# Optimization experiments

Hardware: AMD Instinct MI355X
Metric: run time of the kernel (lower is better)

Reference implementation:

```python
import jax, jax.numpy as jnp
import numpy as np

VTH = 1.0          # firing threshold
SG_ALPHA = 4.0     # surrogate-gradient sharpness
TAU_MEM = 20.0

@jax.custom_vjp
def spike_fn(v):
    # Heaviside spike: 1 where membrane exceeds 0 (v is already v_mem - VTH)
    return (v > 0.0).astype(v.dtype)

def _spike_fwd(v):
    return spike_fn(v), v

def _spike_bwd(v, g):
    # sigmoid surrogate derivative: alpha * s * (1 - s)
    s = jax.nn.sigmoid(SG_ALPHA * v)
    return (g * SG_ALPHA * s * (1.0 - s),)

spike_fn.defvjp(_spike_fwd, _spike_bwd)

def lif_scan(h):
    # h: (batch, time, seq, hidden) -> spikes same shape, rate scalar
    beta = 1.0 - 1.0 / TAU_MEM  # membrane decay
    b, t, s, d = h.shape
    h_t = jnp.moveaxis(h, 1, 0)  # (time, batch, seq, hidden)

    def step(v, inp):
        v = beta * v + inp
        spk = spike_fn(v - VTH)
        v = v * (1.0 - spk)  # hard reset
        return v, spk

    v0 = jnp.zeros((b, s, d), dtype=h.dtype)
    _, spikes = jax.lax.scan(step, v0, h_t)
    spikes = jnp.moveaxis(spikes, 0, 1)  # (batch, time, seq, hidden)
    rate = spikes.mean()
    return spikes, rate

def setup_inputs() -> dict:
    key = jax.random.key(0)
    k1, k2, k3 = jax.random.split(key, 3)
    b, t, s, d = 16, 4, 256, 512
    hidden = 2048
    x = jax.random.normal(k1, (b, t, s, d), dtype=jnp.float32)
    # Kaiming-ish init so membrane inputs are O(1)
    w1 = jax.random.normal(k2, (hidden, d), dtype=jnp.float32) * (1.0 / np.sqrt(d))
    w2 = jax.random.normal(k3, (d, hidden), dtype=jnp.float32) * (1.0 / np.sqrt(hidden))
    return {"x": x, "w1": w1, "w2": w2}

def reference(x, w1, w2):
    # fc1: (b,t,s,d) @ (hidden,d)^T -> (b,t,s,hidden)
    h = jnp.einsum('btsd,hd->btsh', x, w1)
    spikes, rate = lif_scan(h)
    # fc2: (b,t,s,hidden) @ (d,hidden)^T -> (b,t,s,d)
    out = jnp.einsum('btsh,dh->btsd', spikes, w2)
    return out, rate
```

## Files before the change

kernel.cpp:

```cpp
#include <hip/hip_runtime.h>
#include <stdint.h>


typedef __attribute__((ext_vector_type(8))) short short8;
typedef __attribute__((ext_vector_type(4))) float f32x4;

#define AS1 __attribute__((address_space(1)))
#define AS3 __attribute__((address_space(3)))

__device__ __forceinline__ void load_lds16(const void* g, void* l) {
  __builtin_amdgcn_global_load_lds((const AS1 void*)g, (AS3 void*)l, 16, 0, 0);
}

__device__ __forceinline__ unsigned short f2bf(float f) {
  union { float f; unsigned u; } un; un.f = f;
  unsigned r = un.u + 0x7FFF + ((un.u >> 16) & 1);
  return (unsigned short)(r >> 16);
}
__device__ __forceinline__ float bf2f(unsigned short u) {
  union { unsigned u; float f; } un; un.u = ((unsigned)u) << 16; return un.f;
}

__global__ __launch_bounds__(256) void k0_split(
    const float* __restrict__ w2, unsigned short* __restrict__ hi,
    unsigned short* __restrict__ lo)
{
  int i = (blockIdx.x * 256 + threadIdx.x) * 4;
  float4 w = *(const float4*)&w2[i];
  unsigned short h4[4], l4[4];
  float ws[4] = {w.x, w.y, w.z, w.w};
#pragma unroll
  for (int c = 0; c < 4; ++c) {
    unsigned short h = f2bf(ws[c]);
    h4[c] = h;
    l4[c] = f2bf(ws[c] - bf2f(h));
  }
  *(ushort4*)&hi[i] = *(const ushort4*)h4;
  *(ushort4*)&lo[i] = *(const ushort4*)l4;
}

#define K1KT 16
#define SA_STR 176
#define SB_STR 176

__global__ __launch_bounds__(256, 4) void k1_gemm_lif(
    const float* __restrict__ x,
    const float* __restrict__ w1,
    unsigned short* __restrict__ spikes,
    unsigned* __restrict__ cnt_out)
{
  __shared__ float sA[K1KT * SA_STR];
  __shared__ float sB[K1KT * SB_STR];

  const int tid = threadIdx.x;
  const int tx  = tid & 15;
  const int ty  = tid >> 4;

  const int bx = blockIdx.x;
  const int b  = bx >> 3;
  const int s0 = (bx & 7) * 32;
  const int h0 = blockIdx.y * 128;

  const int kg = tid & 3;
  const int u  = tid >> 2;

  float acc[8][8];
#pragma unroll
  for (int m = 0; m < 8; ++m)
#pragma unroll
    for (int j = 0; j < 8; ++j) acc[m][j] = 0.0f;

  const size_t growA0 = ((size_t)(b * 4 + (u & 3)) << 8) + s0 + (u >> 2);
  const size_t growA1 = growA0 + 16;
  const float* xA0 = x  + growA0 * 512 + kg * 4;
  const float* xA1 = x  + growA1 * 512 + kg * 4;
  const float* wB0 = w1 + (size_t)(h0 + u) * 512 + kg * 4;
  const float* wB1 = w1 + (size_t)(h0 + u + 64) * 512 + kg * 4;

  float* sAw = &sA[(4 * kg) * SA_STR + u + 16 * kg];
  float* sBw = &sB[(4 * kg) * SB_STR + u + 16 * kg];

  const float* sAr = &sA[ty * 8];
  const float* sBr = &sB[tx * 4];

  for (int k0 = 0; k0 < 512; k0 += K1KT) {
    float4 a0v = *(const float4*)(xA0 + k0);
    float4 a1v = *(const float4*)(xA1 + k0);
    float4 b0v = *(const float4*)(wB0 + k0);
    float4 b1v = *(const float4*)(wB1 + k0);

    __syncthreads();
    {
      float a0s[4] = {a0v.x, a0v.y, a0v.z, a0v.w};
      float a1s[4] = {a1v.x, a1v.y, a1v.z, a1v.w};
      float b0s[4] = {b0v.x, b0v.y, b0v.z, b0v.w};
      float b1s[4] = {b1v.x, b1v.y, b1v.z, b1v.w};
#pragma unroll
      for (int c = 0; c < 4; ++c) {
        sAw[c * SA_STR]      = a0s[c];
        sAw[c * SA_STR + 64] = a1s[c];
        sBw[c * SB_STR]      = b0s[c];
        sBw[c * SB_STR + 64] = b1s[c];
      }
    }
    __syncthreads();

#pragma unroll
    for (int k = 0; k < K1KT; ++k) {
      const int off = k * SA_STR + 16 * (k >> 2);
      float4 va0 = *(const float4*)(sAr + off);
      float4 va1 = *(const float4*)(sAr + off + 4);
      float4 vb0 = *(const float4*)(sBr + off);
      float4 vb1 = *(const float4*)(sBr + off + 64);
      float av[8] = {va0.x, va0.y, va0.z, va0.w, va1.x, va1.y, va1.z, va1.w};
      float bv[8] = {vb0.x, vb0.y, vb0.z, vb0.w, vb1.x, vb1.y, vb1.z, vb1.w};
#pragma unroll
      for (int m = 0; m < 8; ++m)
#pragma unroll
        for (int j = 0; j < 8; ++j)
          acc[m][j] = __builtin_fmaf(av[m], bv[j], acc[m][j]);
    }
  }

  unsigned cnt = 0;
#pragma unroll
  for (int i = 0; i < 2; ++i) {
    unsigned short sp[4][8];
#pragma unroll
    for (int j = 0; j < 8; ++j) {
      float v = 0.0f;
#pragma unroll
      for (int t = 0; t < 4; ++t) {
        float vv = __fadd_rn(__fmul_rn(0.95f, v), acc[i * 4 + t][j]);
        bool s = vv > 1.0f;
        sp[t][j] = s ? (unsigned short)0x3F80 : (unsigned short)0;
        cnt += s ? 1u : 0u;
        v = s ? 0.0f : vv;
      }
    }
#pragma unroll
    for (int t = 0; t < 4; ++t) {
      size_t grow = ((size_t)(b * 4 + t) << 8) + s0 + ty * 2 + i;
      unsigned short* rowp = spikes + grow * 2048 + h0;
      ushort4 o0, o1;
      o0.x = sp[t][0]; o0.y = sp[t][1]; o0.z = sp[t][2]; o0.w = sp[t][3];
      o1.x = sp[t][4]; o1.y = sp[t][5]; o1.z = sp[t][6]; o1.w = sp[t][7];
      *(ushort4*)&rowp[tx * 4]      = o0;
      *(ushort4*)&rowp[64 + tx * 4] = o1;
    }
  }

#pragma unroll
  for (int off = 32; off; off >>= 1) cnt += __shfl_down(cnt, off);
  if ((tid & 63) == 0) atomicAdd(cnt_out, cnt);
}

__global__ __launch_bounds__(256, 2) void k2_gemm_mfma(
    const unsigned short* __restrict__ spikes,
    const unsigned short* __restrict__ w2h,
    const unsigned short* __restrict__ w2l,
    float* __restrict__ out)
{
  __shared__ alignas(16) short smA [128 * 64];
  __shared__ alignas(16) short smBh[128 * 64];
  __shared__ alignas(16) short smBl[128 * 64];

  const int tid  = threadIdx.x;
  const int lane = tid & 63;
  const int quad = lane >> 4;
  const int l15  = lane & 15;
  const int wv   = tid >> 6;
  const int wm   = wv & 1;
  const int wn   = wv >> 1;

  const size_t r0 = (size_t)blockIdx.x * 128;
  const int    d0 = blockIdx.y * 128;

  int srow[4], sg8[4];
#pragma unroll
  for (int j = 0; j < 4; ++j) {
    int gi  = j * 256 + tid;
    srow[j] = gi >> 3;
    sg8[j]  = ((gi & 7) ^ (srow[j] & 7)) * 8;
  }

  const unsigned short* ab  = spikes + r0 * 2048;
  const unsigned short* bhb = w2h + (size_t)d0 * 2048;
  const unsigned short* blb = w2l + (size_t)d0 * 2048;

  f32x4 acc[4][4] = {};

  for (int k0 = 0; k0 < 2048; k0 += 64) {
    __syncthreads();
#pragma unroll
    for (int j = 0; j < 4; ++j) {
      load_lds16(ab  + (size_t)srow[j] * 2048 + k0 + sg8[j],
                 &smA [(j * 256 + tid) * 8]);
      load_lds16(bhb + (size_t)srow[j] * 2048 + k0 + sg8[j],
                 &smBh[(j * 256 + tid) * 8]);
      load_lds16(blb + (size_t)srow[j] * 2048 + k0 + sg8[j],
                 &smBl[(j * 256 + tid) * 8]);
    }
    __syncthreads();

#pragma unroll
    for (int ks = 0; ks < 2; ++ks) {
      short8 af[4], bh[4], bl[4];
#pragma unroll
      for (int mi = 0; mi < 4; ++mi) {
        int m = wm * 64 + mi * 16 + l15;
        af[mi] = ((const short8*)smA)[m * 8 + ((ks * 4 + quad) ^ (m & 7))];
      }
#pragma unroll
      for (int ni = 0; ni < 4; ++ni) {
        int n = wn * 64 + ni * 16 + l15;
        int sl = n * 8 + ((ks * 4 + quad) ^ (n & 7));
        bh[ni] = ((const short8*)smBh)[sl];
        bl[ni] = ((const short8*)smBl)[sl];
      }
#pragma unroll
      for (int mi = 0; mi < 4; ++mi)
#pragma unroll
        for (int ni = 0; ni < 4; ++ni) {
          acc[mi][ni] = __builtin_amdgcn_mfma_f32_16x16x32_bf16(
              af[mi], bh[ni], acc[mi][ni], 0, 0, 0);
          acc[mi][ni] = __builtin_amdgcn_mfma_f32_16x16x32_bf16(
              af[mi], bl[ni], acc[mi][ni], 0, 0, 0);
        }
    }
  }

  float* ob = out + r0 * 512 + d0;
#pragma unroll
  for (int mi = 0; mi < 4; ++mi)
#pragma unroll
    for (int ni = 0; ni < 4; ++ni)
#pragma unroll
      for (int r = 0; r < 4; ++r) {
        int rr = wm * 64 + mi * 16 + quad * 4 + r;
        int cc = wn * 64 + ni * 16 + l15;
        ob[(size_t)rr * 512 + cc] = acc[mi][ni][r];
      }
}

#define KT 16
#define PADF 68

__global__ __launch_bounds__(256) void k2_gemm_valu(
    const unsigned short* __restrict__ spikes,
    const float* __restrict__ w2,
    float* __restrict__ out)
{
  __shared__ float sA[KT][PADF];
  __shared__ float sB[KT][PADF];

  const int tid = threadIdx.x;
  const int tx  = tid & 15;
  const int ty  = tid >> 4;
  const int lr  = tid >> 2;
  const int lg  = tid & 3;

  const size_t r0 = (size_t)blockIdx.x * 64;
  const int    d0 = blockIdx.y * 64;

  float acc[4][4];
#pragma unroll
  for (int i = 0; i < 4; ++i)
#pragma unroll
    for (int j = 0; j < 4; ++j) acc[i][j] = 0.0f;

  for (int k0 = 0; k0 < 2048; k0 += KT) {
    __syncthreads();
    ushort4 av = *(const ushort4*)&spikes[(r0 + lr) * 2048 + k0 + lg * 4];
    float4  bv = *(const float4*)&w2[(size_t)(d0 + lr) * 2048 + k0 + lg * 4];
    sA[lg * 4 + 0][lr] = bf2f(av.x); sA[lg * 4 + 1][lr] = bf2f(av.y);
    sA[lg * 4 + 2][lr] = bf2f(av.z); sA[lg * 4 + 3][lr] = bf2f(av.w);
    sB[lg * 4 + 0][lr] = bv.x; sB[lg * 4 + 1][lr] = bv.y;
    sB[lg * 4 + 2][lr] = bv.z; sB[lg * 4 + 3][lr] = bv.w;
    __syncthreads();

#pragma unroll
    for (int k = 0; k < KT; ++k) {
      float4 a4 = *(const float4*)&sA[k][ty * 4];
      float4 b4 = *(const float4*)&sB[k][tx * 4];
      float aa[4] = {a4.x, a4.y, a4.z, a4.w};
      float bb[4] = {b4.x, b4.y, b4.z, b4.w};
#pragma unroll
      for (int i = 0; i < 4; ++i)
#pragma unroll
        for (int j = 0; j < 4; ++j)
          acc[i][j] = __builtin_fmaf(aa[i], bb[j], acc[i][j]);
    }
  }

#pragma unroll
  for (int i = 0; i < 4; ++i) {
    float4 o = make_float4(acc[i][0], acc[i][1], acc[i][2], acc[i][3]);
    *(float4*)&out[(r0 + ty * 4 + i) * 512 + d0 + tx * 4] = o;
  }
}

__global__ void k3_rate(const unsigned* __restrict__ cnt, float* __restrict__ dst) {
  dst[0] = (float)((double)(*cnt) / 33554432.0);
}

extern "C" void kernel_launch(void* const* d_in, const int* in_sizes, int n_in,
                              void* d_out, int out_size, void* d_ws, size_t ws_size,
                              hipStream_t stream) {
  const float* x  = (const float*)d_in[0];
  const float* w1 = (const float*)d_in[1];
  const float* w2 = (const float*)d_in[2];
  float* out = (float*)d_out;

  unsigned* cnt = (unsigned*)d_ws;
  unsigned short* spikes = (unsigned short*)((char*)d_ws + 256);
  const size_t SPIKES_B = (size_t)16384 * 2048 * 2;
  unsigned short* w2h = (unsigned short*)((char*)d_ws + 256 + SPIKES_B);
  unsigned short* w2l = w2h + (size_t)512 * 2048;
  const size_t NEED_SPLIT = 256 + SPIKES_B + 2 * (size_t)512 * 2048 * 2;

  hipMemsetAsync(d_ws, 0, 256, stream);

  hipLaunchKernelGGL(k1_gemm_lif, dim3(128, 16), dim3(256), 0, stream,
                     x, w1, spikes, cnt);

  if (ws_size >= NEED_SPLIT) {
    hipLaunchKernelGGL(k0_split, dim3(1024), dim3(256), 0, stream, w2, w2h, w2l);
    hipLaunchKernelGGL(k2_gemm_mfma, dim3(128, 4), dim3(256), 0, stream,
                       spikes, w2h, w2l, out);
  } else {
    hipLaunchKernelGGL(k2_gemm_valu, dim3(256, 8), dim3(256), 0, stream,
                       spikes, w2, out);
  }

  hipLaunchKernelGGL(k3_rate, dim3(1), dim3(1), 0, stream, cnt, out + 8388608);
}
```

Measured before the change: 511.1 us.

## Double-buffer fc2 GEMM LDS tiles with async prefetch and vmcnt waits

Splits the fc2 GEMM's 64-wide K tile into two 32-wide LDS buffers. The next half-tile is issued via global_load_lds while the current one is consumed by MFMAs, and hand-written s_waitcnt vmcnt plus s_barrier sequences replace the two __syncthreads per iteration. The swizzle is adapted to the 4-chunk row layout. This targets the exposed global-load latency between tiles, in exchange for more barriers per K step and reliance on exact vmcnt counting that could race if the compiler reorders memory operations.

```diff
diff --git a/kernel.cpp b/kernel.cpp
--- a/kernel.cpp
+++ b/kernel.cpp
@@ -155,15 +155,61 @@
   if ((tid & 63) == 0) atomicAdd(cnt_out, cnt);
 }
 
+#define K2_ISSUE(K0, SA, SBH, SBL)                                         \
+  do {                                                                     \
+    _Pragma("unroll")                                                      \
+    for (int j = 0; j < 2; ++j) {                                          \
+      load_lds16(ab  + (size_t)srow[j] * 2048 + (K0) + sg8[j],             \
+                 (short*)(SA)  + (j * 256 + tid) * 8);                     \
+      load_lds16(bhb + (size_t)srow[j] * 2048 + (K0) + sg8[j],             \
+                 (short*)(SBH) + (j * 256 + tid) * 8);                     \
+      load_lds16(blb + (size_t)srow[j] * 2048 + (K0) + sg8[j],             \
+                 (short*)(SBL) + (j * 256 + tid) * 8);                     \
+    }                                                                      \
+  } while (0)
+
+#define K2_COMPUTE(SA, SBH, SBL)                                           \
+  do {                                                                     \
+    short8 af[4], bh[4], bl[4];                                            \
+    _Pragma("unroll")                                                      \
+    for (int mi = 0; mi < 4; ++mi) {                                       \
+      int m = wm * 64 + mi * 16 + l15;                                     \
+      af[mi] = ((const short8*)(SA))[m * 4 + (quad ^ ((m >> 1) & 3))];     \
+    }                                                                      \
+    _Pragma("unroll")                                                      \
+    for (int ni = 0; ni < 4; ++ni) {                                       \
+      int n = wn * 64 + ni * 16 + l15;                                     \
+      int sl = n * 4 + (quad ^ ((n >> 1) & 3));                            \
+      bh[ni] = ((const short8*)(SBH))[sl];                                 \
+      bl[ni] = ((const short8*)(SBL))[sl];                                 \
+    }                                                                      \
+    _Pragma("unroll")                                                      \
+    for (int mi = 0; mi < 4; ++mi)                                         \
+      _Pragma("unroll")                                                    \
+      for (int ni = 0; ni < 4; ++ni) {                                     \
+        acc[mi][ni] = __builtin_amdgcn_mfma_f32_16x16x32_bf16(             \
+            af[mi], bh[ni], acc[mi][ni], 0, 0, 0);                         \
+        acc[mi][ni] = __builtin_amdgcn_mfma_f32_16x16x32_bf16(             \
+            af[mi], bl[ni], acc[mi][ni], 0, 0, 0);                         \
+      }                                                                    \
+  } while (0)
+
+#define K2_W6B() asm volatile("s_waitcnt vmcnt(6)\ns_barrier" ::: "memory")
+#define K2_W0B() asm volatile("s_waitcnt vmcnt(0)\ns_barrier" ::: "memory")
+#define K2_LGB() asm volatile("s_waitcnt lgkmcnt(0)\ns_barrier" ::: "memory")
+
 __global__ __launch_bounds__(256, 2) void k2_gemm_mfma(
     const unsigned short* __restrict__ spikes,
     const unsigned short* __restrict__ w2h,
     const unsigned short* __restrict__ w2l,
     float* __restrict__ out)
 {
-  __shared__ alignas(16) short smA [128 * 64];
-  __shared__ alignas(16) short smBh[128 * 64];
-  __shared__ alignas(16) short smBl[128 * 64];
+  __shared__ alignas(16) short smA0 [128 * 32];
+  __shared__ alignas(16) short smBh0[128 * 32];
+  __shared__ alignas(16) short smBl0[128 * 32];
+  __shared__ alignas(16) short smA1 [128 * 32];
+  __shared__ alignas(16) short smBh1[128 * 32];
+  __shared__ alignas(16) short smBl1[128 * 32];
 
   const int tid  = threadIdx.x;
   const int lane = tid & 63;
@@ -176,12 +222,12 @@
   const size_t r0 = (size_t)blockIdx.x * 128;
   const int    d0 = blockIdx.y * 128;
 
-  int srow[4], sg8[4];
-#pragma unroll
-  for (int j = 0; j < 4; ++j) {
+  int srow[2], sg8[2];
+#pragma unroll
+  for (int j = 0; j < 2; ++j) {
     int gi  = j * 256 + tid;
-    srow[j] = gi >> 3;
-    sg8[j]  = ((gi & 7) ^ (srow[j] & 7)) * 8;
+    srow[j] = gi >> 2;
+    sg8[j]  = (((gi & 3) ^ ((srow[j] >> 1) & 3))) * 8;
   }
 
   const unsigned short* ab  = spikes + r0 * 2048;
@@ -190,44 +236,17 @@
 
   f32x4 acc[4][4] = {};
 
+  K2_ISSUE(0, smA0, smBh0, smBl0);
+
   for (int k0 = 0; k0 < 2048; k0 += 64) {
-    __syncthreads();
-#pragma unroll
-    for (int j = 0; j < 4; ++j) {
-      load_lds16(ab  + (size_t)srow[j] * 2048 + k0 + sg8[j],
-                 &smA [(j * 256 + tid) * 8]);
-      load_lds16(bhb + (size_t)srow[j] * 2048 + k0 + sg8[j],
-                 &smBh[(j * 256 + tid) * 8]);
-      load_lds16(blb + (size_t)srow[j] * 2048 + k0 + sg8[j],
-                 &smBl[(j * 256 + tid) * 8]);
-    }
-    __syncthreads();
-
-#pragma unroll
-    for (int ks = 0; ks < 2; ++ks) {
-      short8 af[4], bh[4], bl[4];
-#pragma unroll
-      for (int mi = 0; mi < 4; ++mi) {
-        int m = wm * 64 + mi * 16 + l15;
-        af[mi] = ((const short8*)smA)[m * 8 + ((ks * 4 + quad) ^ (m & 7))];
-      }
-#pragma unroll
-      for (int ni = 0; ni < 4; ++ni) {
-        int n = wn * 64 + ni * 16 + l15;
-        int sl = n * 8 + ((ks * 4 + quad) ^ (n & 7));
-        bh[ni] = ((const short8*)smBh)[sl];
-        bl[ni] = ((const short8*)smBl)[sl];
-      }
-#pragma unroll
-      for (int mi = 0; mi < 4; ++mi)
-#pragma unroll
-        for (int ni = 0; ni < 4; ++ni) {
-          acc[mi][ni] = __builtin_amdgcn_mfma_f32_16x16x32_bf16(
-              af[mi], bh[ni], acc[mi][ni], 0, 0, 0);
-          acc[mi][ni] = __builtin_amdgcn_mfma_f32_16x16x32_bf16(
-              af[mi], bl[ni], acc[mi][ni], 0, 0, 0);
-        }
-    }
+    K2_ISSUE(k0 + 32, smA1, smBh1, smBl1);
+    K2_W6B();
+    K2_COMPUTE(smA0, smBh0, smBl0);
+    K2_LGB();
+    if (k0 < 1984) { K2_ISSUE(k0 + 64, smA0, smBh0, smBl0); K2_W6B(); }
+    else           { K2_W0B(); }
+    K2_COMPUTE(smA1, smBh1, smBl1);
+    if (k0 < 1984) K2_LGB();
   }
 
   float* ob = out + r0 * 512 + d0;
```

After: 542.9 us. 6.2% more time.
